# Optimization experiments

Measured on AMD Instinct MI355X. Metric: run time of the kernel, lower is better.

## Reference

```python
import jax, jax.numpy as jnp
import numpy as np

DIM = 1024
HEADS = 16
BLK = 129
DK = 64
DV = 64
B = 4
N = BLK * 32  # 4128


def setup_inputs() -> dict:
    key = jax.random.key(0)
    ks = jax.random.split(key, 6)
    inner_k = HEADS * DK
    inner_v = HEADS * DV
    s = 1.0 / np.sqrt(DIM)
    x = jax.random.normal(ks[0], (B, N, DIM), dtype=jnp.float32)
    Wq = jax.random.normal(ks[1], (inner_k, DIM), dtype=jnp.float32) * s
    Wk = jax.random.normal(ks[2], (inner_k, DIM), dtype=jnp.float32) * s
    Wv = jax.random.normal(ks[3], (inner_v, DIM), dtype=jnp.float32) * s
    Wo = jax.random.normal(ks[4], (DIM, inner_v), dtype=jnp.float32) * (1.0 / np.sqrt(inner_v))
    bo = jax.random.normal(ks[5], (DIM,), dtype=jnp.float32) * 0.01
    return {"x": x, "Wq": Wq, "Wk": Wk, "Wv": Wv, "Wo": Wo, "bo": bo}


def reference(x, Wq, Wk, Wv, Wo, bo):
    Bsz, Nlen, D = x.shape
    nb = Nlen // BLK
    scale = 1.0 / np.sqrt(DK)
    # projections (Linear without bias: x @ W.T)
    q = (x @ Wq.T).reshape(Bsz, nb, BLK, HEADS, DK)
    k = (x @ Wk.T).reshape(Bsz, nb, BLK, HEADS, DK)
    v = (x @ Wv.T).reshape(Bsz, nb, BLK, HEADS, DV)
    # block-local attention: each block attends within itself
    scores = jnp.einsum('bnqhd,bnkhd->bnhqk', q, k) * scale  # [B,nb,H,BLK,BLK]
    attn = jax.nn.softmax(scores, axis=-1)
    out_blk = jnp.einsum('bnhqk,bnkhd->bnhqd', attn, v)  # [B,nb,H,BLK,DV]
    # global attention among the first token of each block
    qg = q[:, :, 0]  # [B,nb,H,DK]
    kg = k[:, :, 0]
    vg = v[:, :, 0]
    sg = jnp.einsum('bqhd,bkhd->bhqk', qg, kg) * scale  # [B,H,nb,nb]
    ag = jax.nn.softmax(sg, axis=-1)
    out_g = jnp.einsum('bhqk,bkhd->bqhd', ag, vg)  # [B,nb,H,DV]
    # add global output onto position 0 of each block
    out_blk = out_blk.at[:, :, :, 0, :].add(out_g.transpose(0, 1, 2, 3).swapaxes(2, 2))  # out_g already [B,nb,H,DV]
    # reassemble to [B,N,H*DV]
    out = out_blk.transpose(0, 1, 3, 2, 4).reshape(Bsz, Nlen, HEADS * DV)
    return out @ Wo.T + bo
```

## Files before the change

### kernel.cpp

```cpp
#include <hip/hip_runtime.h>

typedef unsigned short u16;
typedef __attribute__((ext_vector_type(8))) __bf16 bf16x8;
typedef __attribute__((ext_vector_type(4))) float f32x4;
typedef __attribute__((ext_vector_type(8))) u16 u16x8;
typedef __attribute__((ext_vector_type(4))) u16 u16x4;

#define DIMSZ 1024
#define HEADS 16
#define BLKSZ 129
#define NBLK 32
#define NTOK (BLKSZ * NBLK)
#define BATCH 4
#define MROWS (BATCH * NTOK)

#define MFMA __builtin_amdgcn_mfma_f32_16x16x32_bf16

#define SSTR 152
#define KSTR 72

#define NKT 32
#define NPH 32

__device__ __forceinline__ float bf2f(u16 u) {
  return __uint_as_float(((unsigned)u) << 16);
}
__device__ __forceinline__ u16 f2bf(float f) {
  unsigned u = __float_as_uint(f);
  u += 0x7FFFu + ((u >> 16) & 1u);
  return (u16)(u >> 16);
}

#define GLD16(ldsp, gp) __builtin_amdgcn_global_load_lds( \
    (const __attribute__((address_space(1))) void*)(gp),   \
    (__attribute__((address_space(3))) void*)(ldsp), 16, 0, 0)

__global__ __launch_bounds__(256) void cast_f32_bf16(
    const float* __restrict__ in, u16* __restrict__ out, int n)
{
  int i = (blockIdx.x * 256 + threadIdx.x) * 4;
  if (i < n) {
    float4 f = *(const float4*)(in + i);
    u16x4 o = { f2bf(f.x), f2bf(f.y), f2bf(f.z), f2bf(f.w) };
    *(u16x4*)(out + i) = o;
  }
}

__global__ __launch_bounds__(256) void cast_w3(
    const float* __restrict__ a, const float* __restrict__ b,
    const float* __restrict__ c, u16* __restrict__ out)
{
  const int nw = DIMSZ * DIMSZ;
  int i = (blockIdx.x * 256 + threadIdx.x) * 4;
  const float* src = (i < nw) ? a : (i < 2 * nw ? b : c);
  int j = (i < nw) ? i : (i < 2 * nw ? i - nw : i - 2 * nw);
  float4 f = *(const float4*)(src + j);
  u16x4 o = { f2bf(f.x), f2bf(f.y), f2bf(f.z), f2bf(f.w) };
  *(u16x4*)(out + i) = o;
}

__device__ __forceinline__ int xcd_swz(int bid, int nwg) {
  const int xcd = bid & 7, l = bid >> 3;
  const int q = nwg >> 3, r = nwg & 7;
  return (xcd < r ? xcd * (q + 1) : r * (q + 1) + (xcd - r) * q) + l;
}

__device__ __forceinline__ void stage_pair(u16* slot, const u16* gA1,
                                           const u16* gB1, int k0, int tid) {
  GLD16(slot + tid * 8, gA1 + k0);
  GLD16(slot + 4096 + tid * 8, gA1 + 128 * DIMSZ + k0);
  GLD16(slot + 8192 + tid * 8, gB1 + k0);
  GLD16(slot + 12288 + tid * 8, gB1 + 128 * DIMSZ + k0);
}

__device__ __forceinline__ void gemm_pipe256(
    const u16* __restrict__ A, const u16* __restrict__ Bm,
    int m0, int n0, int tid, u16 (*sm)[16384], f32x4 (*acc)[4])
{
  const int lane = tid & 63, w = tid >> 6;
  const int qd = lane >> 4, l15 = lane & 15;
  const int wm = (w >> 2) * 128, wn = (w & 3) * 64;
  const int qdsw = (qd ^ ((l15 >> 1) & 3)) * 8;

  const int srow = tid >> 2;
  const int schk = (tid & 3) ^ ((tid >> 3) & 3);
  const u16* gA1 = A + (size_t)(m0 + srow) * DIMSZ + schk * 8;
  const u16* gB1 = Bm + (size_t)(n0 + srow) * DIMSZ + schk * 8;

  stage_pair(sm[0], gA1, gB1, 0, tid);
  stage_pair(sm[1], gA1, gB1, 32, tid);
  asm volatile("s_waitcnt vmcnt(4)" ::: "memory");
  __builtin_amdgcn_s_barrier();
  __builtin_amdgcn_sched_barrier(0);

#pragma unroll 4
  for (int g = 0; g < NPH; ++g) {
    const u16* sA = sm[g & 3];
    const u16* sB = sm[g & 3] + 8192;

    bf16x8 af[8], bv[4];
#pragma unroll
    for (int mi = 0; mi < 8; ++mi)
      af[mi] = *(const bf16x8*)&sA[(wm + mi * 16 + l15) * 32 + qdsw];
#pragma unroll
    for (int ni = 0; ni < 4; ++ni)
      bv[ni] = *(const bf16x8*)&sB[(wn + ni * 16 + l15) * 32 + qdsw];

    if (g + 2 < NPH)
      stage_pair(sm[(g + 2) & 3], gA1, gB1, (g + 2) * 32, tid);

    __builtin_amdgcn_sched_barrier(0);
    __builtin_amdgcn_s_barrier();

    __builtin_amdgcn_s_setprio(1);
#pragma unroll
    for (int mi = 0; mi < 8; ++mi)
#pragma unroll
      for (int ni = 0; ni < 4; ++ni)
        acc[mi][ni] = MFMA(af[mi], bv[ni], acc[mi][ni], 0, 0, 0);
    __builtin_amdgcn_s_setprio(0);
    __builtin_amdgcn_sched_barrier(0);

    if (g + 2 < NPH) {
      asm volatile("s_waitcnt vmcnt(4)" ::: "memory");
    } else if (g + 1 < NPH) {
      asm volatile("s_waitcnt vmcnt(0)" ::: "memory");
    }
    __builtin_amdgcn_s_barrier();
    __builtin_amdgcn_sched_barrier(0);
  }
}

__global__ __launch_bounds__(512, 2) void gemm_qkv(
    const u16* __restrict__ A, const u16* __restrict__ B,
    u16* __restrict__ Cq, u16* __restrict__ Ck, u16* __restrict__ Cv)
{
  __shared__ u16 sm[4][16384];
  const int tid = threadIdx.x;
  f32x4 acc[8][4];
#pragma unroll
  for (int mi = 0; mi < 8; ++mi)
#pragma unroll
    for (int ni = 0; ni < 4; ++ni)
      acc[mi][ni] = (f32x4){0.f, 0.f, 0.f, 0.f};

  const int wg = xcd_swz(blockIdx.x, 65 * 12);
  const int nt = wg % 12, mt = wg / 12;
  const int m0 = mt * 256, n0 = nt * 256;

  gemm_pipe256(A, B, m0, n0, tid, sm, acc);

  u16* C = nt < 4 ? Cq : (nt < 8 ? Ck : Cv);
  const int c0 = (nt & 3) * 256;
  const int lane = tid & 63, w = tid >> 6;
  const int qd = lane >> 4, l15 = lane & 15;
  const int wm = (w >> 2) * 128, wn = (w & 3) * 64;
#pragma unroll
  for (int mi = 0; mi < 8; ++mi)
#pragma unroll
    for (int ni = 0; ni < 4; ++ni) {
      const int row0 = m0 + wm + mi * 16 + qd * 4;
      const int col  = c0 + wn + ni * 16 + l15;
#pragma unroll
      for (int r = 0; r < 4; ++r)
        if (row0 + r < MROWS)
          C[(size_t)(row0 + r) * DIMSZ + col] = f2bf(acc[mi][ni][r]);
    }
}

__device__ __forceinline__ void stage_sq(u16* slot, const u16* gA,
                                         const u16* gB, int tid) {
  GLD16(slot + tid * 8, gA);
  GLD16(slot + 2048 + tid * 8, gA + 64 * DIMSZ);
  GLD16(slot + 4096 + tid * 8, gB);
  GLD16(slot + 6144 + tid * 8, gB + 64 * DIMSZ);
}

__device__ __forceinline__ void gemm_pipe_sq(
    const u16* __restrict__ A, const u16* __restrict__ Bm,
    int m0, int n0, int tid, u16 (*sm)[8192], f32x4 (*acc)[4])
{
  const int lane = tid & 63, w = tid >> 6;
  const int qd = lane >> 4, l15 = lane & 15;
  const int wm = (w >> 1) * 64, wn = (w & 1) * 64;
  const int qdsw = (qd ^ ((l15 >> 1) & 3)) * 8;

  const int srow = tid >> 2;
  const int schk = (tid & 3) ^ ((tid >> 3) & 3);
  const u16* gA = A + (size_t)(m0 + srow) * DIMSZ + schk * 8;
  const u16* gB = Bm + (size_t)(n0 + srow) * DIMSZ + schk * 8;

  u16 *p0 = sm[0], *p1 = sm[1], *p2 = sm[2];

  stage_sq(p0, gA, gB, tid);
  stage_sq(p1, gA + 32, gB + 32, tid);
  asm volatile("s_waitcnt vmcnt(4)" ::: "memory");
  __builtin_amdgcn_s_barrier();
  __builtin_amdgcn_sched_barrier(0);

  for (int t = 0; t < NKT; ++t) {
    if (t + 2 < NKT)
      stage_sq(p2, gA + (t + 2) * 32, gB + (t + 2) * 32, tid);

    bf16x8 af[4], bv[4];
#pragma unroll
    for (int mi = 0; mi < 4; ++mi)
      af[mi] = *(const bf16x8*)&p0[(wm + mi * 16 + l15) * 32 + qdsw];
#pragma unroll
    for (int ni = 0; ni < 4; ++ni)
      bv[ni] = *(const bf16x8*)&p0[4096 + (wn + ni * 16 + l15) * 32 + qdsw];

    __builtin_amdgcn_s_setprio(1);
#pragma unroll
    for (int mi = 0; mi < 4; ++mi)
#pragma unroll
      for (int ni = 0; ni < 4; ++ni)
        acc[mi][ni] = MFMA(af[mi], bv[ni], acc[mi][ni], 0, 0, 0);
    __builtin_amdgcn_s_setprio(0);

    __builtin_amdgcn_sched_barrier(0);
    if (t + 2 < NKT) {
      asm volatile("s_waitcnt vmcnt(4)" ::: "memory");
    } else {
      asm volatile("s_waitcnt vmcnt(0)" ::: "memory");
    }
    __builtin_amdgcn_s_barrier();
    __builtin_amdgcn_sched_barrier(0);

    u16* tmp = p0; p0 = p1; p1 = p2; p2 = tmp;
  }
}

__global__ __launch_bounds__(256, 3) void gemm_out(
    const u16* __restrict__ A, const u16* __restrict__ B,
    float* __restrict__ C, const float* __restrict__ bias)
{
  __shared__ u16 sm[3][8192];
  const int tid = threadIdx.x;
  f32x4 acc[4][4];
#pragma unroll
  for (int mi = 0; mi < 4; ++mi)
#pragma unroll
    for (int ni = 0; ni < 4; ++ni)
      acc[mi][ni] = (f32x4){0.f, 0.f, 0.f, 0.f};

  const int wg = xcd_swz(blockIdx.x, 129 * 8);
  const int nt = wg & 7, mt = wg >> 3;
  const int m0 = mt * 128, n0 = nt * 128;

  gemm_pipe_sq(A, B, m0, n0, tid, sm, acc);

  const int lane = tid & 63, w = tid >> 6;
  const int qd = lane >> 4, l15 = lane & 15;
  const int wm = (w >> 1) * 64, wn = (w & 1) * 64;
#pragma unroll
  for (int mi = 0; mi < 4; ++mi)
#pragma unroll
    for (int ni = 0; ni < 4; ++ni) {
      const int row0 = m0 + wm + mi * 16 + qd * 4;
      const int col  = n0 + wn + ni * 16 + l15;
      float badd = bias[col];
#pragma unroll
      for (int r = 0; r < 4; ++r)
        C[(size_t)(row0 + r) * DIMSZ + col] = acc[mi][ni][r] + badd;
    }
}

__global__ __launch_bounds__(256) void global_attn(
    const u16* __restrict__ q, const u16* __restrict__ k,
    const u16* __restrict__ v, float* __restrict__ g)
{
  __shared__ float sQ[NBLK * 64];
  __shared__ float sKT[64 * NBLK];
  __shared__ float sV[NBLK * 64];
  __shared__ float sp[4][NBLK];
  const int b = blockIdx.x >> 4, h = blockIdx.x & 15;
  const int tid = threadIdx.x, lane = tid & 63, w = tid >> 6;

  for (int idx = tid; idx < NBLK * 64; idx += 256) {
    int j = idx >> 6, d = idx & 63;
    size_t off = ((size_t)(b * NTOK + j * BLKSZ)) * DIMSZ + h * 64 + d;
    sQ[idx] = bf2f(q[off]);
    sKT[d * NBLK + j] = bf2f(k[off]);
    sV[idx] = bf2f(v[off]);
  }
  __syncthreads();

  for (int i = w; i < NBLK; i += 4) {
    float s = -3.0e38f;
    if (lane < 32) {
      float acc = 0.f;
      for (int d = 0; d < 64; ++d) acc += sQ[i * 64 + d] * sKT[d * NBLK + lane];
      s = acc * 0.125f;
    }
    float m = s;
    for (int t = 1; t < 64; t <<= 1) m = fmaxf(m, __shfl_xor(m, t));
    float e = (lane < 32) ? __expf(s - m) : 0.f;
    float sum = e;
    for (int t = 1; t < 64; t <<= 1) sum += __shfl_xor(sum, t);
    if (lane < 32) sp[w][lane] = e / sum;
    asm volatile("s_waitcnt lgkmcnt(0)" ::: "memory");
    float acc = 0.f;
    for (int jj = 0; jj < NBLK; ++jj) acc += sp[w][jj] * sV[jj * 64 + lane];
    g[(((size_t)b * NBLK + i) * HEADS + h) * 64 + lane] = acc;
  }
}

__global__ __launch_bounds__(512) void block_attn(
    const u16* q, const u16* __restrict__ k,
    const u16* __restrict__ v, const float* __restrict__ g,
    u16* ao)
{
  __shared__ u16 sS[144 * SSTR];
  __shared__ u16 sKV[144 * KSTR];
  const int b = blockIdx.x, blk = blockIdx.y, h = blockIdx.z;
  const int tid = threadIdx.x, lane = tid & 63, w = tid >> 6;
  const int qd = lane >> 4, l15 = lane & 15;
  const int h64 = h * 64;
  const size_t row_base = (size_t)b * NTOK + (size_t)blk * BLKSZ;
  const f32x4 zero4 = {0.f, 0.f, 0.f, 0.f};

  {
    const u16x8 zero8 = {0, 0, 0, 0, 0, 0, 0, 0};
    for (int c = tid; c < 144 * 8; c += 512) {
      int row = c >> 3, cc = c & 7;
      u16x8 val = zero8;
      if (row < BLKSZ)
        val = *(const u16x8*)(k + (row_base + row) * DIMSZ + h64 + cc * 8);
      *(u16x8*)&sKV[row * KSTR + cc * 8] = val;
    }
  }
  __syncthreads();

  {
    const int tbeg = w * 10;
    const int tend = (w == 7) ? 81 : tbeg + 10;
    int cur_mt = -1;
    bf16x8 qf0, qf1;
    for (int t = tbeg; t < tend; ++t) {
      int mt = t / 9, nt = t - mt * 9;
      if (mt != cur_mt) {
        cur_mt = mt;
        int qrow = mt * 16 + l15;
        if (qrow > 128) qrow = 128;
        const u16* qp = q + (row_base + qrow) * DIMSZ + h64;
        qf0 = *(const bf16x8*)(qp + qd * 8);
        qf1 = *(const bf16x8*)(qp + 32 + qd * 8);
      }
      bf16x8 kf0 = *(const bf16x8*)&sKV[(nt * 16 + l15) * KSTR + qd * 8];
      bf16x8 kf1 = *(const bf16x8*)&sKV[(nt * 16 + l15) * KSTR + 32 + qd * 8];
      f32x4 c = zero4;
      c = MFMA(qf0, kf0, c, 0, 0, 0);
      c = MFMA(qf1, kf1, c, 0, 0, 0);
      int r0 = mt * 16 + qd * 4, col = nt * 16 + l15;
#pragma unroll
      for (int r = 0; r < 4; ++r)
        sS[(r0 + r) * SSTR + col] = f2bf(c[r] * 0.125f);
    }
  }
  __syncthreads();

  for (int c = tid; c < BLKSZ * 8; c += 512) {
    int row = c >> 3, cc = c & 7;
    u16x8 val = *(const u16x8*)(v + (row_base + row) * DIMSZ + h64 + cc * 8);
#pragma unroll
    for (int jj = 0; jj < 8; ++jj)
      sKV[(cc * 8 + jj) * SSTR + row] = val[jj];
  }

  for (int row = w; row < BLKSZ; row += 8) {
    float x1 = bf2f(sS[row * SSTR + lane]);
    float x2 = bf2f(sS[row * SSTR + 64 + lane]);
    float x3 = (lane == 0) ? bf2f(sS[row * SSTR + 128]) : -3.0e38f;
    float m = fmaxf(fmaxf(x1, x2), x3);
    for (int t = 1; t < 64; t <<= 1) m = fmaxf(m, __shfl_xor(m, t));
    float e1 = __expf(x1 - m), e2 = __expf(x2 - m);
    float e3 = (lane == 0) ? __expf(x3 - m) : 0.f;
    float s = e1 + e2 + e3;
    for (int t = 1; t < 64; t <<= 1) s += __shfl_xor(s, t);
    float inv = 1.f / s;
    sS[row * SSTR + lane] = f2bf(e1 * inv);
    sS[row * SSTR + 64 + lane] = f2bf(e2 * inv);
    if (lane == 0) sS[row * SSTR + 128] = f2bf(e3 * inv);
  }
  __syncthreads();

  for (int t = w; t < 36; t += 8) {
    int mt = t >> 2, nt = t & 3;
    f32x4 c = zero4;
#pragma unroll
    for (int kk = 0; kk < 128; kk += 32) {
      bf16x8 pf = *(const bf16x8*)&sS[(mt * 16 + l15) * SSTR + kk + qd * 8];
      bf16x8 vf = *(const bf16x8*)&sKV[(nt * 16 + l15) * SSTR + kk + qd * 8];
      c = MFMA(pf, vf, c, 0, 0, 0);
    }
    int dv = nt * 16 + l15;
    float v128 = bf2f(sKV[dv * SSTR + 128]);
    int r0 = mt * 16 + qd * 4;
#pragma unroll
    for (int r = 0; r < 4; ++r) {
      int row = r0 + r;
      if (row < BLKSZ) {
        float p128 = bf2f(sS[row * SSTR + 128]);
        float val = c[r] + p128 * v128;
        if (row == 0)
          val += g[(((size_t)b * NBLK + blk) * HEADS + h) * 64 + dv];
        ao[(row_base + row) * DIMSZ + h64 + dv] = f2bf(val);
      }
    }
  }
}

extern "C" void kernel_launch(void* const* d_in, const int* in_sizes, int n_in,
                              void* d_out, int out_size, void* d_ws, size_t ws_size,
                              hipStream_t stream) {
  const float* x  = (const float*)d_in[0];
  const float* Wq = (const float*)d_in[1];
  const float* Wk = (const float*)d_in[2];
  const float* Wv = (const float*)d_in[3];
  const float* Wo = (const float*)d_in[4];
  const float* bo = (const float*)d_in[5];
  float* out = (float*)d_out;

  char* ws = (char*)d_ws;
  const size_t xb = (size_t)MROWS * DIMSZ * sizeof(u16);
  float* gb     = (float*)ws;
  u16*   qb     = (u16*)(ws + (1u << 20));
  u16*   x16    = (u16*)(ws + (1u << 20) + xb);
  u16*   Wqkv16 = (u16*)(ws + (1u << 20) + 2 * xb);
  u16*   Wo16   = x16;
  u16*   kb     = (u16*)d_out;
  u16*   vb     = (u16*)d_out + (size_t)MROWS * DIMSZ;

  const int nx = MROWS * DIMSZ;
  const int nw = DIMSZ * DIMSZ;
  cast_f32_bf16<<<nx / 1024, 256, 0, stream>>>(x, x16, nx);
  cast_w3<<<3 * nw / 1024, 256, 0, stream>>>(Wq, Wk, Wv, Wqkv16);

  gemm_qkv<<<dim3(65 * 12), 512, 0, stream>>>(x16, Wqkv16, qb, kb, vb);

  cast_f32_bf16<<<nw / 1024, 256, 0, stream>>>(Wo, Wo16, nw);

  global_attn<<<dim3(BATCH * HEADS), 256, 0, stream>>>(qb, kb, vb, gb);
  block_attn<<<dim3(BATCH, NBLK, HEADS), 512, 0, stream>>>(qb, kb, vb, gb, qb);
  gemm_out<<<dim3(129 * 8), 256, 0, stream>>>(qb, Wo16, out, bo);
}
```

Measured before the change: 404.6 us.

## Merge input casts, deepen QKV GEMM pipeline with register ping-pong, pack V transpose

The x cast and the three weight casts now run as one launch instead of two. The QKV GEMM drops its per-step double barrier for a 3-stage-ahead LDS prefetch, and it alternates between two register sets so the next step's fragment loads happen in the middle of the current MFMAs. Launch bounds go from (512,2) to (512,1) to allow the extra registers, which may lower occupancy. The V transpose in block attention now writes two rows as one packed 32-bit LDS store.

```diff
diff --git a/kernel.cpp b/kernel.cpp
--- a/kernel.cpp
+++ b/kernel.cpp
@@ -35,6 +35,28 @@
     (const __attribute__((address_space(1))) void*)(gp),   \
     (__attribute__((address_space(3))) void*)(ldsp), 16, 0, 0)
 
+__global__ __launch_bounds__(256) void cast_in(
+    const float* __restrict__ x, const float* __restrict__ wq,
+    const float* __restrict__ wk, const float* __restrict__ wv,
+    u16* __restrict__ x16, u16* __restrict__ w16)
+{
+  const int nx = MROWS * DIMSZ, nw = DIMSZ * DIMSZ;
+  int i = (blockIdx.x * 256 + threadIdx.x) * 4;
+  const float* src;
+  u16* dst;
+  int j;
+  if (i < nx) { src = x; dst = x16; j = i; }
+  else {
+    int k = i - nx;
+    dst = w16; j = k;
+    src = (k < nw) ? wq : (k < 2 * nw ? wk : wv);
+    j = (k < nw) ? k : (k < 2 * nw ? k - nw : k - 2 * nw);
+  }
+  float4 f = *(const float4*)(src + j);
+  u16x4 o = { f2bf(f.x), f2bf(f.y), f2bf(f.z), f2bf(f.w) };
+  *(u16x4*)(dst + (i < nx ? j : (i - nx))) = o;
+}
+
 __global__ __launch_bounds__(256) void cast_f32_bf16(
     const float* __restrict__ in, u16* __restrict__ out, int n)
 {
@@ -44,19 +66,6 @@
     u16x4 o = { f2bf(f.x), f2bf(f.y), f2bf(f.z), f2bf(f.w) };
     *(u16x4*)(out + i) = o;
   }
-}
-
-__global__ __launch_bounds__(256) void cast_w3(
-    const float* __restrict__ a, const float* __restrict__ b,
-    const float* __restrict__ c, u16* __restrict__ out)
-{
-  const int nw = DIMSZ * DIMSZ;
-  int i = (blockIdx.x * 256 + threadIdx.x) * 4;
-  const float* src = (i < nw) ? a : (i < 2 * nw ? b : c);
-  int j = (i < nw) ? i : (i < 2 * nw ? i - nw : i - 2 * nw);
-  float4 f = *(const float4*)(src + j);
-  u16x4 o = { f2bf(f.x), f2bf(f.y), f2bf(f.z), f2bf(f.w) };
-  *(u16x4*)(out + i) = o;
 }
 
 __device__ __forceinline__ int xcd_swz(int bid, int nwg) {
@@ -73,88 +82,93 @@
   GLD16(slot + 12288 + tid * 8, gB1 + 128 * DIMSZ + k0);
 }
 
-__device__ __forceinline__ void gemm_pipe256(
-    const u16* __restrict__ A, const u16* __restrict__ Bm,
-    int m0, int n0, int tid, u16 (*sm)[16384], f32x4 (*acc)[4])
-{
+#define RD8(slot, row, sw) (*(const bf16x8*)&(slot)[(row) * 32 + (sw)])
+
+__global__ __launch_bounds__(512, 1) void gemm_qkv(
+    const u16* __restrict__ A, const u16* __restrict__ B,
+    u16* __restrict__ Cq, u16* __restrict__ Ck, u16* __restrict__ Cv)
+{
+  __shared__ u16 sm[4][16384];
+  const int tid = threadIdx.x;
   const int lane = tid & 63, w = tid >> 6;
   const int qd = lane >> 4, l15 = lane & 15;
   const int wm = (w >> 2) * 128, wn = (w & 3) * 64;
   const int qdsw = (qd ^ ((l15 >> 1) & 3)) * 8;
 
+  f32x4 acc[8][4];
+#pragma unroll
+  for (int mi = 0; mi < 8; ++mi)
+#pragma unroll
+    for (int ni = 0; ni < 4; ++ni)
+      acc[mi][ni] = (f32x4){0.f, 0.f, 0.f, 0.f};
+
+  const int wg = xcd_swz(blockIdx.x, 65 * 12);
+  const int nt = wg % 12, mt = wg / 12;
+  const int m0 = mt * 256, n0 = nt * 256;
+
   const int srow = tid >> 2;
   const int schk = (tid & 3) ^ ((tid >> 3) & 3);
   const u16* gA1 = A + (size_t)(m0 + srow) * DIMSZ + schk * 8;
-  const u16* gB1 = Bm + (size_t)(n0 + srow) * DIMSZ + schk * 8;
+  const u16* gB1 = B + (size_t)(n0 + srow) * DIMSZ + schk * 8;
 
   stage_pair(sm[0], gA1, gB1, 0, tid);
   stage_pair(sm[1], gA1, gB1, 32, tid);
+  stage_pair(sm[2], gA1, gB1, 64, tid);
   asm volatile("s_waitcnt vmcnt(4)" ::: "memory");
   __builtin_amdgcn_s_barrier();
   __builtin_amdgcn_sched_barrier(0);
 
-#pragma unroll 4
-  for (int g = 0; g < NPH; ++g) {
-    const u16* sA = sm[g & 3];
-    const u16* sB = sm[g & 3] + 8192;
-
-    bf16x8 af[8], bv[4];
-#pragma unroll
-    for (int mi = 0; mi < 8; ++mi)
-      af[mi] = *(const bf16x8*)&sA[(wm + mi * 16 + l15) * 32 + qdsw];
-#pragma unroll
-    for (int ni = 0; ni < 4; ++ni)
-      bv[ni] = *(const bf16x8*)&sB[(wn + ni * 16 + l15) * 32 + qdsw];
-
-    if (g + 2 < NPH)
-      stage_pair(sm[(g + 2) & 3], gA1, gB1, (g + 2) * 32, tid);
-
-    __builtin_amdgcn_sched_barrier(0);
-    __builtin_amdgcn_s_barrier();
-
-    __builtin_amdgcn_s_setprio(1);
-#pragma unroll
-    for (int mi = 0; mi < 8; ++mi)
-#pragma unroll
-      for (int ni = 0; ni < 4; ++ni)
-        acc[mi][ni] = MFMA(af[mi], bv[ni], acc[mi][ni], 0, 0, 0);
-    __builtin_amdgcn_s_setprio(0);
-    __builtin_amdgcn_sched_barrier(0);
-
-    if (g + 2 < NPH) {
-      asm volatile("s_waitcnt vmcnt(4)" ::: "memory");
-    } else if (g + 1 < NPH) {
-      asm volatile("s_waitcnt vmcnt(0)" ::: "memory");
-    }
-    __builtin_amdgcn_s_barrier();
-    __builtin_amdgcn_sched_barrier(0);
-  }
-}
-
-__global__ __launch_bounds__(512, 2) void gemm_qkv(
-    const u16* __restrict__ A, const u16* __restrict__ B,
-    u16* __restrict__ Cq, u16* __restrict__ Ck, u16* __restrict__ Cv)
-{
-  __shared__ u16 sm[4][16384];
-  const int tid = threadIdx.x;
-  f32x4 acc[8][4];
-#pragma unroll
-  for (int mi = 0; mi < 8; ++mi)
-#pragma unroll
-    for (int ni = 0; ni < 4; ++ni)
-      acc[mi][ni] = (f32x4){0.f, 0.f, 0.f, 0.f};
-
-  const int wg = xcd_swz(blockIdx.x, 65 * 12);
-  const int nt = wg % 12, mt = wg / 12;
-  const int m0 = mt * 256, n0 = nt * 256;
-
-  gemm_pipe256(A, B, m0, n0, tid, sm, acc);
+  bf16x8 afLa[4], bva[4], afLb[4], bvb[4], afH[4];
+#pragma unroll
+  for (int mi = 0; mi < 4; ++mi) afLa[mi] = RD8(sm[0], wm + mi * 16 + l15, qdsw);
+#pragma unroll
+  for (int ni = 0; ni < 4; ++ni) bva[ni] = RD8(sm[0] + 8192, wn + ni * 16 + l15, qdsw);
+
+#define QSTEP(T, AC, BC, AN, BN)                                              \
+  {                                                                           \
+    const u16* slc = sm[(T) & 3];                                             \
+    if ((T) + 3 < NPH)                                                        \
+      stage_pair(sm[((T) + 3) & 3], gA1, gB1, ((T) + 3) * 32, tid);           \
+    _Pragma("unroll")                                                         \
+    for (int mi = 0; mi < 4; ++mi)                                            \
+      afH[mi] = RD8(slc, wm + 64 + mi * 16 + l15, qdsw);                      \
+    _Pragma("unroll")                                                         \
+    for (int mi = 0; mi < 4; ++mi)                                            \
+      _Pragma("unroll")                                                       \
+      for (int ni = 0; ni < 4; ++ni)                                          \
+        acc[mi][ni] = MFMA(AC[mi], BC[ni], acc[mi][ni], 0, 0, 0);             \
+    if ((T) + 1 < NPH) {                                                      \
+      const u16* sln = sm[((T) + 1) & 3];                                     \
+      _Pragma("unroll")                                                       \
+      for (int mi = 0; mi < 4; ++mi)                                          \
+        AN[mi] = RD8(sln, wm + mi * 16 + l15, qdsw);                          \
+      _Pragma("unroll")                                                       \
+      for (int ni = 0; ni < 4; ++ni)                                          \
+        BN[ni] = RD8(sln + 8192, wn + ni * 16 + l15, qdsw);                   \
+    }                                                                         \
+    _Pragma("unroll")                                                         \
+    for (int mi = 0; mi < 4; ++mi)                                            \
+      _Pragma("unroll")                                                       \
+      for (int ni = 0; ni < 4; ++ni)                                          \
+        acc[mi + 4][ni] = MFMA(afH[mi], BC[ni], acc[mi + 4][ni], 0, 0, 0);    \
+    __builtin_amdgcn_sched_barrier(0);                                        \
+    if ((T) + 3 < NPH) {                                                      \
+      asm volatile("s_waitcnt vmcnt(4)" ::: "memory");                        \
+    } else {                                                                  \
+      asm volatile("s_waitcnt vmcnt(0)" ::: "memory");                        \
+    }                                                                         \
+    __builtin_amdgcn_s_barrier();                                             \
+    __builtin_amdgcn_sched_barrier(0);                                        \
+  }
+
+  for (int t = 0; t < NPH; t += 2) {
+    QSTEP(t, afLa, bva, afLb, bvb);
+    QSTEP(t + 1, afLb, bvb, afLa, bva);
+  }
+#undef QSTEP
 
   u16* C = nt < 4 ? Cq : (nt < 8 ? Ck : Cv);
   const int c0 = (nt & 3) * 256;
-  const int lane = tid & 63, w = tid >> 6;
-  const int qd = lane >> 4, l15 = lane & 15;
-  const int wm = (w >> 2) * 128, wn = (w & 3) * 64;
 #pragma unroll
   for (int mi = 0; mi < 8; ++mi)
 #pragma unroll
@@ -360,12 +374,22 @@
   }
   __syncthreads();
 
-  for (int c = tid; c < BLKSZ * 8; c += 512) {
-    int row = c >> 3, cc = c & 7;
-    u16x8 val = *(const u16x8*)(v + (row_base + row) * DIMSZ + h64 + cc * 8);
-#pragma unroll
-    for (int jj = 0; jj < 8; ++jj)
-      sKV[(cc * 8 + jj) * SSTR + row] = val[jj];
+  {
+    int c = tid;
+    int p = c >> 3, cc = c & 7;
+    u16x8 v0 = *(const u16x8*)(v + (row_base + 2 * p) * DIMSZ + h64 + cc * 8);
+    u16x8 v1 = *(const u16x8*)(v + (row_base + 2 * p + 1) * DIMSZ + h64 + cc * 8);
+#pragma unroll
+    for (int jj = 0; jj < 8; ++jj) {
+      unsigned pack = (unsigned)v0[jj] | ((unsigned)v1[jj] << 16);
+      *(unsigned*)&sKV[(cc * 8 + jj) * SSTR + 2 * p] = pack;
+    }
+    if (tid < 8) {
+      u16x8 vl = *(const u16x8*)(v + (row_base + 128) * DIMSZ + h64 + tid * 8);
+#pragma unroll
+      for (int jj = 0; jj < 8; ++jj)
+        sKV[(tid * 8 + jj) * SSTR + 128] = vl[jj];
+    }
   }
 
   for (int row = w; row < BLKSZ; row += 8) {
@@ -434,8 +458,7 @@
 
   const int nx = MROWS * DIMSZ;
   const int nw = DIMSZ * DIMSZ;
-  cast_f32_bf16<<<nx / 1024, 256, 0, stream>>>(x, x16, nx);
-  cast_w3<<<3 * nw / 1024, 256, 0, stream>>>(Wq, Wk, Wv, Wqkv16);
+  cast_in<<<(nx + 3 * nw) / 1024, 256, 0, stream>>>(x, Wq, Wk, Wv, x16, Wqkv16);
 
   gemm_qkv<<<dim3(65 * 12), 512, 0, stream>>>(x16, Wqkv16, qb, kb, vb);
 
```

Result: faster. 394.5 us (-2.5%).
